# Optimization experiments

Hardware: AMD Instinct MI355X
Metric: run time of the kernel (lower is better)

Reference implementation:

```python
import math
import jax
import jax.numpy as jnp
import numpy as np

LMAX = 6                 # lmax
F8, F2 = 16, 64          # f_out//8, f_out//2 for f_out=128
DIM6 = sum((2 * l + 1) ** 2 for l in range(LMAX + 1))  # 455 = dim of so3_irreps(6)
NA = NB = NG = 16        # SO(3) activation grid (alpha, beta, gamma)
B, T, H, C = 32, 16, 4, 128


def _real_sh(lmax, xyz):
    # real spherical harmonics: (N,3) unit vectors -> (N,(lmax+1)^2), m=-l..l per l
    x, y, z = xyz[:, 0], xyz[:, 1], xyz[:, 2]
    st = np.sqrt(np.clip(1.0 - z * z, 0.0, None))
    phi = np.arctan2(y, x)
    n = xyz.shape[0]
    P = np.zeros((lmax + 1, lmax + 1, n))
    P[0, 0] = 1.0
    for m in range(1, lmax + 1):
        P[m, m] = -(2 * m - 1) * st * P[m - 1, m - 1]
    for m in range(lmax):
        P[m + 1, m] = (2 * m + 1) * z * P[m, m]
    for m in range(lmax + 1):
        for l in range(m + 2, lmax + 1):
            P[l, m] = ((2 * l - 1) * z * P[l - 1, m] - (l + m - 1) * P[l - 2, m]) / (l - m)
    cols = []
    for l in range(lmax + 1):
        for m in range(-l, l + 1):
            am = abs(m)
            K = math.sqrt((2 * l + 1) / (4 * math.pi) * math.factorial(l - am) / math.factorial(l + am))
            if m > 0:
                cols.append(math.sqrt(2.0) * K * np.cos(m * phi) * P[l, m])
            elif m < 0:
                cols.append(math.sqrt(2.0) * K * np.sin(am * phi) * P[l, am])
            else:
                cols.append(K * P[l, 0])
    return np.stack(cols, axis=-1)


def _flat_wigner(lmax, Rs):
    # component-normalized flat real Wigner-D basis: (G,3,3) -> (G, sum_l (2l+1)^2)
    # D_l(R) solved from Y_l(R x) = D_l(R) Y_l(x) by least squares in float64
    rng = np.random.default_rng(0)
    pts = rng.normal(size=(32, 3))
    pts /= np.linalg.norm(pts, axis=1, keepdims=True)
    Y = _real_sh(lmax, pts)                                     # (32,(lmax+1)^2)
    rp = np.einsum('gij,nj->gni', Rs, pts).reshape(-1, 3)
    Yr = _real_sh(lmax, rp).reshape(len(Rs), 32, -1)            # (G,32,(lmax+1)^2)
    blocks = []
    for l in range(lmax + 1):
        d = 2 * l + 1
        o = l * l
        Apinv = np.linalg.pinv(Y[:, o:o + d])                   # (d,32)
        D = np.einsum('kn,gnm->gmk', Apinv, Yr[:, :, o:o + d])  # (G,d,d)
        blocks.append(math.sqrt(d) * D.reshape(len(Rs), d * d))
    return np.concatenate(blocks, axis=-1)


def _rz(a):
    c, s = np.cos(a), np.sin(a)
    z, o = np.zeros_like(a), np.ones_like(a)
    return np.stack([np.stack([c, -s, z], -1), np.stack([s, c, z], -1), np.stack([z, z, o], -1)], -2)


def _ry(a):
    c, s = np.cos(a), np.sin(a)
    z, o = np.zeros_like(a), np.ones_like(a)
    return np.stack([np.stack([c, z, s], -1), np.stack([z, o, z], -1), np.stack([-s, z, c], -1)], -2)


def _so3_grid():
    # ZYZ Euler grid, Gauss-Legendre in beta; rotations (G,3,3) + Haar weights (G,) summing to 1
    nodes, wts = np.polynomial.legendre.leggauss(NB)
    betas = np.arccos(nodes)
    alphas = np.arange(NA) * 2 * np.pi / NA
    gammas = np.arange(NG) * 2 * np.pi / NG
    Aa, Bb, Cg = np.meshgrid(alphas, betas, gammas, indexing='ij')
    Rs = _rz(Aa.ravel()) @ _ry(Bb.ravel()) @ _rz(Cg.ravel())
    w = np.broadcast_to(wts[None, :, None], (NA, NB, NG)).ravel().copy()
    w *= (2 * np.pi / NA) * (2 * np.pi / NG) / (8 * np.pi ** 2)
    return Rs, w


def _ico_rotations():
    # the 60 rotations of the icosahedral group, generated by closure
    phi = (1.0 + 5.0 ** 0.5) / 2.0
    def rot(axis, ang):
        a = np.asarray(axis, dtype=np.float64)
        a = a / np.linalg.norm(a)
        K = np.array([[0.0, -a[2], a[1]], [a[2], 0.0, -a[0]], [-a[1], a[0], 0.0]])
        return np.eye(3) + math.sin(ang) * K + (1.0 - math.cos(ang)) * (K @ K)
    gens = [rot([0.0, 1.0, phi], 2.0 * np.pi / 5.0), rot([0.0, 0.0, 1.0], np.pi)]
    elems = [np.eye(3)]
    seen = {tuple(np.round(np.eye(3), 5).ravel())}
    frontier = list(elems)
    while frontier:
        nxt = []
        for R in frontier:
            for g in gens:
                Q = g @ R
                k = tuple(np.round(Q, 5).ravel())
                if k not in seen:
                    seen.add(k)
                    elems.append(Q)
                    nxt.append(Q)
        frontier = nxt
    return np.stack(elems)


def _equi_linear(xl, wl):
    # e3nn-style per-irrep linear: xl (...,f_in,u,m), wl (f_in,f_out,u,v); fan_in = f_in*u
    fan_in = wl.shape[0] * wl.shape[2]
    return jnp.einsum('...fum,fguv->...gvm', xl, wl) / np.sqrt(fan_in)


def _forward(x, trajectory, w1s, w1v, w2, D_in, D_outw, ico_wigners):
    b, t, _ = trajectory.shape
    # pack '1x0e+3x1e': scalar = traj[...,9], vectors = traj[...,:9]
    s = trajectory[..., 9][..., None, None, None]       # (b,t,f=1,u=1,m=1)
    v = trajectory[..., :9].reshape(b, t, 1, 3, 3)      # (b,t,f=1,u=3,m=3)
    h = jnp.concatenate([_equi_linear(s, w1s).reshape(b, t, F8, 1),
                         _equi_linear(v, w1v).reshape(b, t, F8, 9)], axis=-1)  # (b,t,16,10)
    # SO(3) activation: coeffs -> grid signal -> relu -> coeffs (lmax 1 -> 6)
    sig = jax.nn.relu(jnp.einsum('btci,gi->btcg', h, D_in))
    h = jnp.einsum('btcg,gi->btci', sig, D_outw)        # (b,t,16,455)
    # per-l equivariant linear, f 16 -> 64
    outs = []
    o = 0
    for l in range(LMAX + 1):
        d = 2 * l + 1
        xl = h[..., o:o + d * d].reshape(b, t, F8, d, d)
        outs.append(_equi_linear(xl, w2[l]).reshape(b, t, F2, d * d))
        o += d * d
    traj = jnp.concatenate(outs, axis=-1)               # (b,t,64,455)
    traj = jnp.einsum('bhcj,ij->bhci', traj, ico_wigners)  # sample on ico rotations
    xg = jnp.einsum('bhcj,ij->bhci', x, ico_wigners)
    return xg, traj


def setup_inputs():
    key = jax.random.key(0)
    ks = jax.random.split(key, 11)
    Rs, w = _so3_grid()
    D_in = _flat_wigner(1, Rs).astype(np.float32)                      # (G,10)
    D_outw = (_flat_wigner(LMAX, Rs) * w[:, None]).astype(np.float32)  # (G,455)
    ico = _flat_wigner(LMAX, _ico_rotations()).astype(np.float32)      # (60,455)
    inp = dict(
        x=jax.random.normal(ks[0], (B, H, C, DIM6), jnp.float32),
        trajectory=jax.random.normal(ks[1], (B, T, 10), jnp.float32),
        w1s=jax.random.normal(ks[2], (1, F8, 1, 1), jnp.float32),
        w1v=jax.random.normal(ks[3], (1, F8, 3, 3), jnp.float32),
        D_in=jnp.asarray(D_in),
        D_outw=jnp.asarray(D_outw),
        ico_wigners=jnp.asarray(ico),
    )
    for l in range(LMAX + 1):
        inp['w2_%d' % l] = jax.random.normal(ks[4 + l], (F8, F2, 2 * l + 1, 2 * l + 1), jnp.float32)
    return inp


def reference(x, trajectory, w1s, w1v, w2_0, w2_1, w2_2, w2_3, w2_4, w2_5, w2_6, D_in, D_outw, ico_wigners):
    w2 = [w2_0, w2_1, w2_2, w2_3, w2_4, w2_5, w2_6]
    return _forward(x, trajectory, w1s, w1v, w2, D_in, D_outw, ico_wigners)
```

## Files before the change

### kernel.cpp

```cpp
#include <hip/hip_runtime.h>
#include <math.h>


#define NBT  512
#define F8c  16
#define F2c  64
#define GJ   455
#define GG   4096
#define NICO 60
#define JP   512

typedef short bf16x8 __attribute__((ext_vector_type(8)));
typedef float f32x4  __attribute__((ext_vector_type(4)));
typedef unsigned int u32;
typedef unsigned short ushort;

struct W7 { const float* p[7]; };

__device__ __forceinline__ ushort f2bf(float f) {
  u32 u = __float_as_uint(f);
  return (ushort)((u + 0x7fffu + ((u >> 16) & 1u)) >> 16);
}

__device__ __forceinline__ int sel7(int l, int a0, int a1, int a2, int a3,
                                    int a4, int a5, int a6) {
  int r = a6;
  r = (l == 5) ? a5 : r; r = (l == 4) ? a4 : r; r = (l == 3) ? a3 : r;
  r = (l == 2) ? a2 : r; r = (l == 1) ? a1 : r; r = (l == 0) ? a0 : r;
  return r;
}
__device__ __forceinline__ float sel7f(int l, float a0, float a1, float a2,
                                       float a3, float a4, float a5, float a6) {
  float r = a6;
  r = (l == 5) ? a5 : r; r = (l == 4) ? a4 : r; r = (l == 3) ? a3 : r;
  r = (l == 2) ? a2 : r; r = (l == 1) ? a1 : r; r = (l == 0) ? a0 : r;
  return r;
}

__global__ __launch_bounds__(256) void k_pre(const float* __restrict__ traj,
                                             const float* __restrict__ w1s,
                                             const float* __restrict__ w1v,
                                             const float* __restrict__ ico,
                                             const float* __restrict__ Dout,
                                             W7 w2,
                                             float* __restrict__ h,
                                             ushort* __restrict__ icoB,
                                             ushort* __restrict__ icoBx,
                                             ushort* __restrict__ DoutBT,
                                             ushort* __restrict__ Abuf,
                                             ushort* __restrict__ Bbuf) {
  __shared__ float t[64][65];
  int b = blockIdx.x, tid = threadIdx.x;
  if (b < 2240) {
    ((uint4*)Abuf)[b * 256 + tid] = (uint4){0, 0, 0, 0};
  } else if (b < 2752) {
    int b2 = b - 2240;
    int jt = b2 & 7, kt = b2 >> 3;
    int tx = tid & 63, ty = tid >> 6;
    #pragma unroll
    for (int i = 0; i < 16; ++i) {
      int r = i * 4 + ty, j = jt * 64 + tx;
      t[r][tx] = (j < GJ) ? Dout[(size_t)(kt * 64 + r) * GJ + j] : 0.f;
    }
    __syncthreads();
    #pragma unroll
    for (int i = 0; i < 16; ++i) {
      int jl = i * 4 + ty;
      DoutBT[(size_t)(jt * 64 + jl) * GG + kt * 64 + tx] = f2bf(t[tx][jl]);
    }
  } else if (b < 4992) {
    int ee = (b - 2752) * 256 + tid;
    if (ee < 573440) {
      int l = (ee >= 4096) + (ee >= 16384) + (ee >= 57344) + (ee >= 114688) +
              (ee >= 225280) + (ee >= 360448);
      int base = sel7(l, 0, 4096, 16384, 57344, 114688, 225280, 360448);
      int d    = sel7(l, 1, 3, 5, 7, 9, 11, 13);
      int Kp   = sel7(l, 64, 64, 128, 128, 192, 192, 256);
      int local = ee - base;
      int row = local / Kp, kcol = local - row * Kp;
      int g2 = row / d, v = row - g2 * d;
      ushort val = 0;
      if (kcol < 16 * d) {
        int f = kcol / d, u = kcol - f * d;
        const float* wl = w2.p[l];
        float scl = rsqrtf(16.f * (float)d);
        val = f2bf(wl[(((size_t)f * 64 + g2) * d + u) * d + v] * scl);
      }
      Bbuf[ee] = val;
    }
  } else if (b < 5312) {
    int idx = (b - 4992) * 256 + tid;
    if (idx < NBT * 160) {
      int bt = idx / 160, r = idx % 160, c = r / 10, i = r % 10;
      const float* tr = traj + bt * 10;
      float val;
      if (i == 0) {
        val = tr[9] * w1s[c];
      } else {
        int k = i - 1, v = k / 3, m = k % 3;
        float s = 0.f;
        #pragma unroll
        for (int u = 0; u < 3; ++u) s = fmaf(tr[u * 3 + m], w1v[c * 9 + u * 3 + v], s);
        val = s * 0.57735026918962576f;
      }
      h[idx] = val;
    }
  } else if (b < 5440) {
    int e = (b - 5312) * 256 + tid;
    int i = e >> 9, k = e & 511;
    ushort val = 0;
    if (i < NICO && k < GJ) {
      int l = (k >= 1) + (k >= 10) + (k >= 35) + (k >= 84) + (k >= 165) + (k >= 286);
      int o = sel7(l, 0, 1, 10, 35, 84, 165, 286);
      int d = sel7(l, 1, 3, 5, 7, 9, 11, 13);
      float rcpd = sel7f(l, 1.f, 1.f / 3.f, 0.2f, 1.f / 7.f, 1.f / 9.f,
                         1.f / 11.f, 1.f / 13.f);
      int local = k - o;
      int m = (int)(((float)local + 0.5f) * rcpd);
      int v = local - m * d;
      val = f2bf(ico[i * GJ + o + v * d + m]);
    }
    icoB[e] = val;
  } else {
    int e = (b - 5440) * 256 + tid;
    int i = e >> 9, j = e & 511;
    icoBx[e] = (i < NICO && j < GJ) ? f2bf(ico[i * GJ + j]) : (ushort)0;
  }
}

__global__ __launch_bounds__(256) void k_sig(const float* __restrict__ h,
                                             const float* __restrict__ Din,
                                             ushort* __restrict__ sigb) {
  __shared__ float hs[160];
  int tid = threadIdx.x;
  int mb = blockIdx.y;
  int kt = blockIdx.x;
  if (tid < 160) hs[tid] = h[mb * 160 + tid];
  float dr[80];
  const float4* dp = (const float4*)(Din + (size_t)(kt * 2048 + tid * 8) * 10);
  #pragma unroll
  for (int q = 0; q < 20; ++q) {
    float4 v = dp[q];
    dr[q * 4 + 0] = v.x; dr[q * 4 + 1] = v.y; dr[q * 4 + 2] = v.z; dr[q * 4 + 3] = v.w;
  }
  __syncthreads();
  #pragma unroll
  for (int r = 0; r < 16; ++r) {
    float hv[10];
    #pragma unroll
    for (int i = 0; i < 10; ++i) hv[i] = hs[r * 10 + i];
    bf16x8 o;
    #pragma unroll
    for (int j = 0; j < 8; ++j) {
      float s = 0.f;
      #pragma unroll
      for (int i = 0; i < 10; ++i) s = fmaf(hv[i], dr[j * 10 + i], s);
      o[j] = (short)f2bf(fmaxf(s, 0.f));
    }
    *(bf16x8*)&sigb[((size_t)(mb * 16 + r)) * GG + kt * 2048 + tid * 8] = o;
  }
}

__global__ __launch_bounds__(256) void k_mm2s(const ushort* __restrict__ A,
                                              const ushort* __restrict__ Bm,
                                              float* __restrict__ part) {
  __shared__ __align__(16) short Asb[2][128 * 64];
  __shared__ __align__(16) short Bsb[2][128 * 64];
  int tid = threadIdx.x;
  int lane = tid & 63, wid = tid >> 6;
  int quad = lane >> 4, lr = lane & 15;
  int wm = wid >> 1, wn = wid & 1;
  int bid = blockIdx.x;
  int mb = bid & 63;
  int split = (bid >> 6) & 1;
  int nb = bid >> 7;
  int k0 = split * 2048;

  const ushort* Ab = A + (size_t)mb * 128 * GG + k0;
  const ushort* Bb = Bm + (size_t)nb * 128 * GG + k0;

  f32x4 acc[4][4];
  #pragma unroll
  for (int a = 0; a < 4; ++a)
    #pragma unroll
    for (int b = 0; b < 4; ++b) acc[a][b] = (f32x4){0.f, 0.f, 0.f, 0.f};

  auto stage = [&](int buf, int kc) {
    #pragma unroll
    for (int it = 0; it < 4; ++it) {
      int s0 = (wid * 4 + it) * 64;
      int s = s0 + lane;
      int r = s >> 3, pp = s & 7, p = pp ^ (r & 7);
      __builtin_amdgcn_global_load_lds(
          (const __attribute__((address_space(1))) u32*)(Ab + (size_t)r * GG + kc + p * 8),
          (__attribute__((address_space(3))) u32*)(&Asb[buf][s0 * 8]), 16, 0, 0);
    }
    #pragma unroll
    for (int it = 0; it < 4; ++it) {
      int s0 = (wid * 4 + it) * 64;
      int s = s0 + lane;
      int r = s >> 3, pp = s & 7, p = pp ^ (r & 7);
      __builtin_amdgcn_global_load_lds(
          (const __attribute__((address_space(1))) u32*)(Bb + (size_t)r * GG + kc + p * 8),
          (__attribute__((address_space(3))) u32*)(&Bsb[buf][s0 * 8]), 16, 0, 0);
    }
  };

  stage(0, 0);
  __syncthreads();
  for (int it = 0; it < 32; ++it) {
    int cur = it & 1;
    if (it < 31) stage(cur ^ 1, (it + 1) * 64);
    #pragma unroll
    for (int ks = 0; ks < 2; ++ks) {
      bf16x8 af[4], bv[4];
      #pragma unroll
      for (int mt = 0; mt < 4; ++mt) {
        int ra = wm * 64 + mt * 16 + lr;
        int v = (ks * 4 + quad) ^ (ra & 7);
        af[mt] = *(const bf16x8*)&Asb[cur][(ra * 8 + v) * 8];
      }
      #pragma unroll
      for (int nt = 0; nt < 4; ++nt) {
        int rb = wn * 64 + nt * 16 + lr;
        int v = (ks * 4 + quad) ^ (rb & 7);
        bv[nt] = *(const bf16x8*)&Bsb[cur][(rb * 8 + v) * 8];
      }
      #pragma unroll
      for (int mt = 0; mt < 4; ++mt)
        #pragma unroll
        for (int nt = 0; nt < 4; ++nt)
          acc[mt][nt] = __builtin_amdgcn_mfma_f32_16x16x32_bf16(af[mt], bv[nt], acc[mt][nt], 0, 0, 0);
    }
    __syncthreads();
  }
  #pragma unroll
  for (int mt = 0; mt < 4; ++mt)
    #pragma unroll
    for (int nt = 0; nt < 4; ++nt) {
      int j = nb * 128 + wn * 64 + nt * 16 + lr;
      #pragma unroll
      for (int r = 0; r < 4; ++r) {
        int m = mb * 128 + wm * 64 + mt * 16 + quad * 4 + r;
        part[((size_t)split * 8192 + m) * 512 + j] = acc[mt][nt][r];
      }
    }
}

__global__ __launch_bounds__(256) void k_red(const float* __restrict__ part,
                                             ushort* __restrict__ Abuf) {
  int t = blockIdx.x * 256 + threadIdx.x;
  int e0 = t * 8;
  int m = e0 >> 9, j0 = e0 & 511;
  const float4* p0 = (const float4*)(part + (size_t)m * 512 + j0);
  const float4* p1 = (const float4*)(part + (size_t)(8192 + m) * 512 + j0);
  float4 a0 = p0[0], a1 = p0[1], b0 = p1[0], b1 = p1[1];
  float s[8] = {a0.x + b0.x, a0.y + b0.y, a0.z + b0.z, a0.w + b0.w,
                a1.x + b1.x, a1.y + b1.y, a1.z + b1.z, a1.w + b1.w};
  int btg = m >> 4, f = m & 15;
  #pragma unroll
  for (int jj = 0; jj < 8; ++jj) {
    int j = j0 + jj;
    if (j < GJ) {
      int l = (j >= 1) + (j >= 10) + (j >= 35) + (j >= 84) + (j >= 165) + (j >= 286);
      int o    = sel7(l, 0, 1, 10, 35, 84, 165, 286);
      int d    = sel7(l, 1, 3, 5, 7, 9, 11, 13);
      int Kp   = sel7(l, 64, 64, 128, 128, 192, 192, 256);
      int Aoff = sel7(l, 0, 32768, 131072, 458752, 917504, 1802240, 2883584);
      float rcpd = sel7f(l, 1.f, 1.f / 3.f, 0.2f, 1.f / 7.f, 1.f / 9.f,
                         1.f / 11.f, 1.f / 13.f);
      int jl = j - o;
      int u = (int)(((float)jl + 0.5f) * rcpd);
      int mB = jl - u * d;
      Abuf[(size_t)Aoff + ((size_t)btg * d + mB) * Kp + f * d + u] = f2bf(s[jj]);
    }
  }
}

__global__ __launch_bounds__(256) void k_mm2f(const ushort* __restrict__ A,
                                              const ushort* __restrict__ Bm,
                                              ushort* __restrict__ Abuf) {
  __shared__ __align__(16) short Asb[2][128 * 64];
  __shared__ __align__(16) short Bsb[2][128 * 64];
  int tid = threadIdx.x;
  int lane = tid & 63, wid = tid >> 6;
  int quad = lane >> 4, lr = lane & 15;
  int wm = wid >> 1, wn = wid & 1;
  int bid = blockIdx.x;
  int mb = bid & 63, nb = bid >> 6;
  f32x4 acc[4][4];
  #pragma unroll
  for (int a = 0; a < 4; ++a)
    #pragma unroll
    for (int b = 0; b < 4; ++b) acc[a][b] = (f32x4){0.f, 0.f, 0.f, 0.f};
  const ushort* Ab = A + (size_t)mb * 128 * GG;
  const ushort* Bb = Bm + (size_t)nb * 128 * GG;
  auto stage = [&](int buf, int kc) {
    #pragma unroll
    for (int it = 0; it < 4; ++it) {
      int s0 = (wid * 4 + it) * 64;
      int s = s0 + lane;
      int r = s >> 3, pp = s & 7, p = pp ^ (r & 7);
      __builtin_amdgcn_global_load_lds(
          (const __attribute__((address_space(1))) u32*)(Ab + (size_t)r * GG + kc + p * 8),
          (__attribute__((address_space(3))) u32*)(&Asb[buf][s0 * 8]), 16, 0, 0);
    }
    #pragma unroll
    for (int it = 0; it < 4; ++it) {
      int s0 = (wid * 4 + it) * 64;
      int s = s0 + lane;
      int r = s >> 3, pp = s & 7, p = pp ^ (r & 7);
      __builtin_amdgcn_global_load_lds(
          (const __attribute__((address_space(1))) u32*)(Bb + (size_t)r * GG + kc + p * 8),
          (__attribute__((address_space(3))) u32*)(&Bsb[buf][s0 * 8]), 16, 0, 0);
    }
  };
  stage(0, 0);
  __syncthreads();
  for (int it = 0; it < 64; ++it) {
    int cur = it & 1;
    if (it < 63) stage(cur ^ 1, (it + 1) * 64);
    #pragma unroll
    for (int ks = 0; ks < 2; ++ks) {
      bf16x8 af[4], bvv[4];
      #pragma unroll
      for (int mt = 0; mt < 4; ++mt) {
        int ra = wm * 64 + mt * 16 + lr;
        int v = (ks * 4 + quad) ^ (ra & 7);
        af[mt] = *(const bf16x8*)&Asb[cur][(ra * 8 + v) * 8];
      }
      #pragma unroll
      for (int nt = 0; nt < 4; ++nt) {
        int rb = wn * 64 + nt * 16 + lr;
        int v = (ks * 4 + quad) ^ (rb & 7);
        bvv[nt] = *(const bf16x8*)&Bsb[cur][(rb * 8 + v) * 8];
      }
      #pragma unroll
      for (int mt = 0; mt < 4; ++mt)
        #pragma unroll
        for (int nt = 0; nt < 4; ++nt)
          acc[mt][nt] = __builtin_amdgcn_mfma_f32_16x16x32_bf16(af[mt], bvv[nt], acc[mt][nt], 0, 0, 0);
    }
    __syncthreads();
  }
  #pragma unroll
  for (int nt = 0; nt < 4; ++nt) {
    int j = nb * 128 + wn * 64 + nt * 16 + lr;
    if (j < GJ) {
      int l = (j >= 1) + (j >= 10) + (j >= 35) + (j >= 84) + (j >= 165) + (j >= 286);
      int o    = sel7(l, 0, 1, 10, 35, 84, 165, 286);
      int d    = sel7(l, 1, 3, 5, 7, 9, 11, 13);
      int Kp   = sel7(l, 64, 64, 128, 128, 192, 192, 256);
      int Aoff = sel7(l, 0, 32768, 131072, 458752, 917504, 1802240, 2883584);
      int jl = j - o;
      float rcpd = 1.0f / (float)d;
      int u = (int)(((float)jl + 0.5f) * rcpd);
      int mB = jl - u * d;
      #pragma unroll
      for (int mt = 0; mt < 4; ++mt)
        #pragma unroll
        for (int r = 0; r < 4; ++r) {
          int m = mb * 128 + wm * 64 + mt * 16 + quad * 4 + r;
          int btg = m >> 4, f = m & 15;
          Abuf[(size_t)Aoff + ((size_t)btg * d + mB) * Kp + f * d + u] =
              f2bf(acc[mt][nt][r]);
        }
    }
  }
}

__global__ __launch_bounds__(256) void k_batchX(const ushort* __restrict__ Abuf,
                                                const ushort* __restrict__ Bbuf,
                                                const float* __restrict__ x,
                                                const ushort* __restrict__ icoBx,
                                                ushort* __restrict__ trajbf,
                                                float* __restrict__ xg) {
  __shared__ __align__(16) short As[2][128 * 64];
  __shared__ __align__(16) short Bs[2][128 * 64];
  int bid = blockIdx.x;
  int tid = threadIdx.x;
  int lane = tid & 63, wid = tid >> 6;
  int quad = lane >> 4, lr = lane & 15;
  int wm = wid >> 1, wn = wid & 1;
  f32x4 acc[4][4];
  #pragma unroll
  for (int a = 0; a < 4; ++a)
    #pragma unroll
    for (int b = 0; b < 4; ++b) acc[a][b] = (f32x4){0.f, 0.f, 0.f, 0.f};

  if (bid >= 1008) {
    int mtile = bid - 1008;
    auto loadx = [&](int itk, float* xv) {
      #pragma unroll
      for (int g = 0; g < 4; ++g) {
        int s = g * 256 + tid;
        int r = s >> 3, p8 = s & 7, p = p8 ^ (r & 7);
        const float* xr = x + (size_t)(mtile * 128 + r) * GJ;
        int j0 = itk * 64 + p * 8;
        #pragma unroll
        for (int jj = 0; jj < 8; ++jj) {
          int j = j0 + jj;
          xv[g * 8 + jj] = (j < GJ) ? xr[j] : 0.f;
        }
      }
    };
    auto writex = [&](int buf, const float* xv) {
      #pragma unroll
      for (int g = 0; g < 4; ++g) {
        int s = g * 256 + tid;
        bf16x8 v8;
        #pragma unroll
        for (int jj = 0; jj < 8; ++jj) v8[jj] = (short)f2bf(xv[g * 8 + jj]);
        *(bf16x8*)&As[buf][s * 8] = v8;
      }
    };
    auto stageBx = [&](int buf, int kc) {
      #pragma unroll
      for (int it = 0; it < 2; ++it) {
        int s0 = (wid * 2 + it) * 64;
        int s = s0 + lane;
        int r = s >> 3, p8 = s & 7, p = p8 ^ (r & 7);
        const ushort* gb = icoBx + (size_t)r * JP + kc + p * 8;
        __builtin_amdgcn_global_load_lds(
            (const __attribute__((address_space(1))) u32*)gb,
            (__attribute__((address_space(3))) u32*)(&Bs[buf][s0 * 8]), 16, 0, 0);
      }
    };
    float xv[32];
    loadx(0, xv);
    writex(0, xv);
    stageBx(0, 0);
    __syncthreads();
    for (int it = 0; it < 8; ++it) {
      int cur = it & 1;
      float xn[32];
      if (it < 7) {
        loadx(it + 1, xn);
        stageBx(cur ^ 1, (it + 1) * 64);
      }
      #pragma unroll
      for (int ks = 0; ks < 2; ++ks) {
        bf16x8 af[4], bv[2];
        #pragma unroll
        for (int mt = 0; mt < 4; ++mt) {
          int ra = wm * 64 + mt * 16 + lr;
          int v = (ks * 4 + quad) ^ (ra & 7);
          af[mt] = *(const bf16x8*)&As[cur][(ra * 8 + v) * 8];
        }
        #pragma unroll
        for (int nt = 0; nt < 2; ++nt) {
          int rb = wn * 32 + nt * 16 + lr;
          int v = (ks * 4 + quad) ^ (rb & 7);
          bv[nt] = *(const bf16x8*)&Bs[cur][(rb * 8 + v) * 8];
        }
        #pragma unroll
        for (int mt = 0; mt < 4; ++mt)
          #pragma unroll
          for (int nt = 0; nt < 2; ++nt)
            acc[mt][nt] = __builtin_amdgcn_mfma_f32_16x16x32_bf16(af[mt], bv[nt], acc[mt][nt], 0, 0, 0);
      }
      if (it < 7) writex(cur ^ 1, xn);
      __syncthreads();
    }
    #pragma unroll
    for (int mt = 0; mt < 4; ++mt)
      #pragma unroll
      for (int nt = 0; nt < 2; ++nt) {
        int i = wn * 32 + nt * 16 + lr;
        if (i < NICO) {
          #pragma unroll
          for (int r = 0; r < 4; ++r) {
            int row = mtile * 128 + wm * 64 + mt * 16 + quad * 4 + r;
            xg[(size_t)row * NICO + i] = acc[mt][nt][r];
          }
        }
      }
    return;
  }

  int l = (bid >= 4) + (bid >= 28) + (bid >= 88) + (bid >= 200) +
          (bid >= 380) + (bid >= 644);
  int bbase = sel7(l, 0, 4, 28, 88, 200, 380, 644);
  int d     = sel7(l, 1, 3, 5, 7, 9, 11, 13);
  int Kp    = sel7(l, 64, 64, 128, 128, 192, 192, 256);
  int o     = sel7(l, 0, 1, 10, 35, 84, 165, 286);
  int Aoff  = sel7(l, 0, 32768, 131072, 458752, 917504, 1802240, 2883584);
  int Boff  = sel7(l, 0, 4096, 16384, 57344, 114688, 225280, 360448);
  int ntc   = sel7(l, 1, 2, 3, 4, 5, 6, 7);
  float rcpntc = sel7f(l, 1.f, 0.5f, 1.f / 3.f, 0.25f, 0.2f, 1.f / 6.f, 1.f / 7.f);
  float rcpd   = sel7f(l, 1.f, 1.f / 3.f, 0.2f, 1.f / 7.f, 1.f / 9.f,
                       1.f / 11.f, 1.f / 13.f);
  int t = bid - bbase;
  int mtile = (int)(((float)t + 0.5f) * rcpntc);
  int ntile = t - mtile * ntc;
  int Nl = 64 * d;

  const ushort* Ab = Abuf + Aoff + (size_t)mtile * 128 * Kp;
  const ushort* Bb = Bbuf + Boff + (size_t)ntile * 128 * Kp;

  auto stage = [&](int buf, int kc) {
    #pragma unroll
    for (int it = 0; it < 4; ++it) {
      int s0 = (wid * 4 + it) * 64;
      int s = s0 + lane;
      int r = s >> 3, pp = s & 7, p = pp ^ (r & 7);
      __builtin_amdgcn_global_load_lds(
          (const __attribute__((address_space(1))) u32*)(Ab + (size_t)r * Kp + kc + p * 8),
          (__attribute__((address_space(3))) u32*)(&As[buf][s0 * 8]), 16, 0, 0);
    }
    #pragma unroll
    for (int it = 0; it < 4; ++it) {
      int s0 = (wid * 4 + it) * 64;
      int s = s0 + lane;
      int r = s >> 3, pp = s & 7, p = pp ^ (r & 7);
      __builtin_amdgcn_global_load_lds(
          (const __attribute__((address_space(1))) u32*)(Bb + (size_t)r * Kp + kc + p * 8),
          (__attribute__((address_space(3))) u32*)(&Bs[buf][s0 * 8]), 16, 0, 0);
    }
  };

  int nIter = Kp >> 6;
  stage(0, 0);
  __syncthreads();
  for (int it = 0; it < nIter; ++it) {
    int cur = it & 1;
    if (it + 1 < nIter) stage(cur ^ 1, (it + 1) * 64);
    #pragma unroll
    for (int ks = 0; ks < 2; ++ks) {
      bf16x8 af[4], bv[4];
      #pragma unroll
      for (int mt = 0; mt < 4; ++mt) {
        int ra = wm * 64 + mt * 16 + lr;
        int v = (ks * 4 + quad) ^ (ra & 7);
        af[mt] = *(const bf16x8*)&As[cur][(ra * 8 + v) * 8];
      }
      #pragma unroll
      for (int nt = 0; nt < 4; ++nt) {
        int rb = wn * 64 + nt * 16 + lr;
        int v = (ks * 4 + quad) ^ (rb & 7);
        bv[nt] = *(const bf16x8*)&Bs[cur][(rb * 8 + v) * 8];
      }
      #pragma unroll
      for (int mt = 0; mt < 4; ++mt)
        #pragma unroll
        for (int nt = 0; nt < 4; ++nt)
          acc[mt][nt] = __builtin_amdgcn_mfma_f32_16x16x32_bf16(af[mt], bv[nt], acc[mt][nt], 0, 0, 0);
    }
    __syncthreads();
  }
  #pragma unroll
  for (int nt = 0; nt < 4; ++nt) {
    int Ncol = ntile * 128 + wn * 64 + nt * 16 + lr;
    if (Ncol < Nl) {
      int g2 = (int)(((float)Ncol + 0.5f) * rcpd);
      int v = Ncol - g2 * d;
      #pragma unroll
      for (int mt = 0; mt < 4; ++mt)
        #pragma unroll
        for (int r = 0; r < 4; ++r) {
          int Mrow = mtile * 128 + wm * 64 + mt * 16 + quad * 4 + r;
          int bt = (int)(((float)Mrow + 0.5f) * rcpd);
          int m = Mrow - bt * d;
          trajbf[(size_t)(bt * 64 + g2) * JP + o + m * d + v] = f2bf(acc[mt][nt][r]);
        }
    }
  }
}

__global__ __launch_bounds__(256) void k_icoT(const ushort* __restrict__ trajbf,
                                              const ushort* __restrict__ icoB,
                                              float* __restrict__ trajo) {
  __shared__ __align__(16) short As[2][128 * 64];
  __shared__ __align__(16) short Bs[2][64 * 64];
  int mtile = blockIdx.x;
  int tid = threadIdx.x;
  int lane = tid & 63, wid = tid >> 6;
  int quad = lane >> 4, lr = lane & 15;
  int wm = wid >> 1, wn = wid & 1;
  f32x4 acc[4][2];
  #pragma unroll
  for (int a = 0; a < 4; ++a)
    #pragma unroll
    for (int b = 0; b < 2; ++b) acc[a][b] = (f32x4){0.f, 0.f, 0.f, 0.f};

  auto stage = [&](int buf, int kc) {
    #pragma unroll
    for (int it = 0; it < 4; ++it) {
      int s0 = (wid * 4 + it) * 64;
      int s = s0 + lane;
      int r = s >> 3, p8 = s & 7, p = p8 ^ (r & 7);
      const ushort* ga = trajbf + (size_t)(mtile * 128 + r) * JP + kc + p * 8;
      __builtin_amdgcn_global_load_lds(
          (const __attribute__((address_space(1))) u32*)ga,
          (__attribute__((address_space(3))) u32*)(&As[buf][s0 * 8]), 16, 0, 0);
    }
    #pragma unroll
    for (int it = 0; it < 2; ++it) {
      int s0 = (wid * 2 + it) * 64;
      int s = s0 + lane;
      int r = s >> 3, p8 = s & 7, p = p8 ^ (r & 7);
      const ushort* gb = icoB + (size_t)r * JP + kc + p * 8;
      __builtin_amdgcn_global_load_lds(
          (const __attribute__((address_space(1))) u32*)gb,
          (__attribute__((address_space(3))) u32*)(&Bs[buf][s0 * 8]), 16, 0, 0);
    }
  };

  stage(0, 0);
  __syncthreads();
  for (int it = 0; it < 8; ++it) {
    int cur = it & 1;
    if (it < 7) stage(cur ^ 1, (it + 1) * 64);
    #pragma unroll
    for (int ks = 0; ks < 2; ++ks) {
      bf16x8 af[4], bv[2];
      #pragma unroll
      for (int mt = 0; mt < 4; ++mt) {
        int ra = wm * 64 + mt * 16 + lr;
        int v = (ks * 4 + quad) ^ (ra & 7);
        af[mt] = *(const bf16x8*)&As[cur][(ra * 8 + v) * 8];
      }
      #pragma unroll
      for (int nt = 0; nt < 2; ++nt) {
        int rb = wn * 32 + nt * 16 + lr;
        int v = (ks * 4 + quad) ^ (rb & 7);
        bv[nt] = *(const bf16x8*)&Bs[cur][(rb * 8 + v) * 8];
      }
      #pragma unroll
      for (int mt = 0; mt < 4; ++mt)
        #pragma unroll
        for (int nt = 0; nt < 2; ++nt)
          acc[mt][nt] = __builtin_amdgcn_mfma_f32_16x16x32_bf16(af[mt], bv[nt], acc[mt][nt], 0, 0, 0);
    }
    __syncthreads();
  }
  #pragma unroll
  for (int mt = 0; mt < 4; ++mt)
    #pragma unroll
    for (int nt = 0; nt < 2; ++nt) {
      int i = wn * 32 + nt * 16 + lr;
      if (i < NICO) {
        #pragma unroll
        for (int r = 0; r < 4; ++r) {
          int row = mtile * 128 + wm * 64 + mt * 16 + quad * 4 + r;
          trajo[(size_t)row * NICO + i] = acc[mt][nt][r];
        }
      }
    }
}

extern "C" void kernel_launch(void* const* d_in, const int* in_sizes, int n_in,
                              void* d_out, int out_size, void* d_ws, size_t ws_size,
                              hipStream_t stream) {
  const float *x = nullptr, *traj = nullptr, *w1s = nullptr, *w1v = nullptr;
  const float *Din = nullptr, *Dout = nullptr, *ico = nullptr;
  W7 w2{};
  for (int i = 0; i < n_in; ++i) {
    const float* p = (const float*)d_in[i];
    switch (in_sizes[i]) {
      case 7454720: x = p; break;
      case 5120:    traj = p; break;
      case 16:      w1s = p; break;
      case 144:     w1v = p; break;
      case 40960:   Din = p; break;
      case 1863680: Dout = p; break;
      case 27300:   ico = p; break;
      case 1024:    w2.p[0] = p; break;
      case 9216:    w2.p[1] = p; break;
      case 25600:   w2.p[2] = p; break;
      case 50176:   w2.p[3] = p; break;
      case 82944:   w2.p[4] = p; break;
      case 123904:  w2.p[5] = p; break;
      case 173056:  w2.p[6] = p; break;
      default: break;
    }
  }
  char* wsb = (char*)d_ws;
  float*  h       = (float*)wsb;
  ushort* DoutBT  = (ushort*)(wsb + 327680);
  ushort* icoB    = (ushort*)(wsb + 4521984);
  ushort* icoBx   = (ushort*)(wsb + 4587520);
  ushort* Abuf    = (ushort*)(wsb + 4653056);
  ushort* Bbuf    = (ushort*)(wsb + 13828096);
  ushort* sigb    = (ushort*)(wsb + 14974976);
  ushort* trajbf  = sigb;
  float*  part    = (float*)(wsb + 82083840);
  float* xg    = (float*)d_out;
  float* trajo = (float*)d_out + 983040;

  k_pre<<<dim3(5568), dim3(256), 0, stream>>>(traj, w1s, w1v, ico, Dout, w2,
                                              h, icoB, icoBx, DoutBT, Abuf, Bbuf);
  k_sig<<<dim3(2, 512), dim3(256), 0, stream>>>(h, Din, sigb);
  if (ws_size >= 115638272ULL) {
    k_mm2s<<<dim3(512),  dim3(256), 0, stream>>>(sigb, DoutBT, part);
    k_red <<<dim3(2048), dim3(256), 0, stream>>>(part, Abuf);
  } else {
    k_mm2f<<<dim3(256),  dim3(256), 0, stream>>>(sigb, DoutBT, Abuf);
  }
  k_batchX<<<dim3(1136), dim3(256), 0, stream>>>(Abuf, Bbuf, x, icoBx, trajbf, xg);
  k_icoT  <<<dim3(256),  dim3(256), 0, stream>>>(trajbf, icoB, trajo);
}
```

Measured before the change: 236.0 us.

## Split x projection into bf16 conversion pass and GEMM merged into icoT kernel

The x×ico GEMM tail blocks in k_batchX, which converted fp32 x to bf16 in registers while computing, become lightweight conversion blocks that write bf16 x to a workspace buffer. The GEMM itself moves into k_icoT as 128 extra blocks that share the async global_load_lds staging path with the trajectory GEMM. The aim is to stop long GEMM tail blocks from extending k_batchX and to reuse the more efficient staged pipeline. In exchange it adds an extra bf16 round trip of x through memory and enlarges the workspace.

```diff
diff --git a/kernel.cpp b/kernel.cpp
--- a/kernel.cpp
+++ b/kernel.cpp
@@ -372,13 +372,27 @@
 __global__ __launch_bounds__(256) void k_batchX(const ushort* __restrict__ Abuf,
                                                 const ushort* __restrict__ Bbuf,
                                                 const float* __restrict__ x,
-                                                const ushort* __restrict__ icoBx,
                                                 ushort* __restrict__ trajbf,
-                                                float* __restrict__ xg) {
+                                                ushort* __restrict__ xbf) {
   __shared__ __align__(16) short As[2][128 * 64];
   __shared__ __align__(16) short Bs[2][128 * 64];
   int bid = blockIdx.x;
   int tid = threadIdx.x;
+
+  if (bid >= 1008) {
+    int e0 = ((bid - 1008) * 256 + tid) * 8;
+    int row = e0 >> 9, j0 = e0 & 511;
+    const float* xr = x + (size_t)row * GJ;
+    bf16x8 v8;
+    #pragma unroll
+    for (int jj = 0; jj < 8; ++jj) {
+      int j = j0 + jj;
+      v8[jj] = (j < GJ) ? (short)f2bf(xr[j]) : (short)0;
+    }
+    *(bf16x8*)&xbf[(size_t)row * JP + j0] = v8;
+    return;
+  }
+
   int lane = tid & 63, wid = tid >> 6;
   int quad = lane >> 4, lr = lane & 15;
   int wm = wid >> 1, wn = wid & 1;
@@ -387,96 +401,6 @@
   for (int a = 0; a < 4; ++a)
     #pragma unroll
     for (int b = 0; b < 4; ++b) acc[a][b] = (f32x4){0.f, 0.f, 0.f, 0.f};
-
-  if (bid >= 1008) {
-    int mtile = bid - 1008;
-    auto loadx = [&](int itk, float* xv) {
-      #pragma unroll
-      for (int g = 0; g < 4; ++g) {
-        int s = g * 256 + tid;
-        int r = s >> 3, p8 = s & 7, p = p8 ^ (r & 7);
-        const float* xr = x + (size_t)(mtile * 128 + r) * GJ;
-        int j0 = itk * 64 + p * 8;
-        #pragma unroll
-        for (int jj = 0; jj < 8; ++jj) {
-          int j = j0 + jj;
-          xv[g * 8 + jj] = (j < GJ) ? xr[j] : 0.f;
-        }
-      }
-    };
-    auto writex = [&](int buf, const float* xv) {
-      #pragma unroll
-      for (int g = 0; g < 4; ++g) {
-        int s = g * 256 + tid;
-        bf16x8 v8;
-        #pragma unroll
-        for (int jj = 0; jj < 8; ++jj) v8[jj] = (short)f2bf(xv[g * 8 + jj]);
-        *(bf16x8*)&As[buf][s * 8] = v8;
-      }
-    };
-    auto stageBx = [&](int buf, int kc) {
-      #pragma unroll
-      for (int it = 0; it < 2; ++it) {
-        int s0 = (wid * 2 + it) * 64;
-        int s = s0 + lane;
-        int r = s >> 3, p8 = s & 7, p = p8 ^ (r & 7);
-        const ushort* gb = icoBx + (size_t)r * JP + kc + p * 8;
-        __builtin_amdgcn_global_load_lds(
-            (const __attribute__((address_space(1))) u32*)gb,
-            (__attribute__((address_space(3))) u32*)(&Bs[buf][s0 * 8]), 16, 0, 0);
-      }
-    };
-    float xv[32];
-    loadx(0, xv);
-    writex(0, xv);
-    stageBx(0, 0);
-    __syncthreads();
-    for (int it = 0; it < 8; ++it) {
-      int cur = it & 1;
-      float xn[32];
-      if (it < 7) {
-        loadx(it + 1, xn);
-        stageBx(cur ^ 1, (it + 1) * 64);
-      }
-      #pragma unroll
-      for (int ks = 0; ks < 2; ++ks) {
-        bf16x8 af[4], bv[2];
-        #pragma unroll
-        for (int mt = 0; mt < 4; ++mt) {
-          int ra = wm * 64 + mt * 16 + lr;
-          int v = (ks * 4 + quad) ^ (ra & 7);
-          af[mt] = *(const bf16x8*)&As[cur][(ra * 8 + v) * 8];
-        }
-        #pragma unroll
-        for (int nt = 0; nt < 2; ++nt) {
-          int rb = wn * 32 + nt * 16 + lr;
-          int v = (ks * 4 + quad) ^ (rb & 7);
-          bv[nt] = *(const bf16x8*)&Bs[cur][(rb * 8 + v) * 8];
-        }
-        #pragma unroll
-        for (int mt = 0; mt < 4; ++mt)
-          #pragma unroll
-          for (int nt = 0; nt < 2; ++nt)
-            acc[mt][nt] = __builtin_amdgcn_mfma_f32_16x16x32_bf16(af[mt], bv[nt], acc[mt][nt], 0, 0, 0);
-      }
-      if (it < 7) writex(cur ^ 1, xn);
-      __syncthreads();
-    }
-    #pragma unroll
-    for (int mt = 0; mt < 4; ++mt)
-      #pragma unroll
-      for (int nt = 0; nt < 2; ++nt) {
-        int i = wn * 32 + nt * 16 + lr;
-        if (i < NICO) {
-          #pragma unroll
-          for (int r = 0; r < 4; ++r) {
-            int row = mtile * 128 + wm * 64 + mt * 16 + quad * 4 + r;
-            xg[(size_t)row * NICO + i] = acc[mt][nt][r];
-          }
-        }
-      }
-    return;
-  }
 
   int l = (bid >= 4) + (bid >= 28) + (bid >= 88) + (bid >= 200) +
           (bid >= 380) + (bid >= 644);
@@ -569,14 +493,30 @@
 
 __global__ __launch_bounds__(256) void k_icoT(const ushort* __restrict__ trajbf,
                                               const ushort* __restrict__ icoB,
-                                              float* __restrict__ trajo) {
+                                              const ushort* __restrict__ xbf,
+                                              const ushort* __restrict__ icoBx,
+                                              float* __restrict__ trajo,
+                                              float* __restrict__ xg) {
   __shared__ __align__(16) short As[2][128 * 64];
   __shared__ __align__(16) short Bs[2][64 * 64];
-  int mtile = blockIdx.x;
+  int bid = blockIdx.x;
   int tid = threadIdx.x;
   int lane = tid & 63, wid = tid >> 6;
   int quad = lane >> 4, lr = lane & 15;
   int wm = wid >> 1, wn = wid & 1;
+
+  const ushort* Ap; const ushort* Bp; float* outp;
+  if (bid < 256) {
+    Ap = trajbf + (size_t)bid * 128 * JP;
+    Bp = icoB;
+    outp = trajo + (size_t)bid * 128 * NICO;
+  } else {
+    int m2 = bid - 256;
+    Ap = xbf + (size_t)m2 * 128 * JP;
+    Bp = icoBx;
+    outp = xg + (size_t)m2 * 128 * NICO;
+  }
+
   f32x4 acc[4][2];
   #pragma unroll
   for (int a = 0; a < 4; ++a)
@@ -589,7 +529,7 @@
       int s0 = (wid * 4 + it) * 64;
       int s = s0 + lane;
       int r = s >> 3, p8 = s & 7, p = p8 ^ (r & 7);
-      const ushort* ga = trajbf + (size_t)(mtile * 128 + r) * JP + kc + p * 8;
+      const ushort* ga = Ap + (size_t)r * JP + kc + p * 8;
       __builtin_amdgcn_global_load_lds(
           (const __attribute__((address_space(1))) u32*)ga,
           (__attribute__((address_space(3))) u32*)(&As[buf][s0 * 8]), 16, 0, 0);
@@ -599,7 +539,7 @@
       int s0 = (wid * 2 + it) * 64;
       int s = s0 + lane;
       int r = s >> 3, p8 = s & 7, p = p8 ^ (r & 7);
-      const ushort* gb = icoB + (size_t)r * JP + kc + p * 8;
+      const ushort* gb = Bp + (size_t)r * JP + kc + p * 8;
       __builtin_amdgcn_global_load_lds(
           (const __attribute__((address_space(1))) u32*)gb,
           (__attribute__((address_space(3))) u32*)(&Bs[buf][s0 * 8]), 16, 0, 0);
@@ -642,8 +582,8 @@
       if (i < NICO) {
         #pragma unroll
         for (int r = 0; r < 4; ++r) {
-          int row = mtile * 128 + wm * 64 + mt * 16 + quad * 4 + r;
-          trajo[(size_t)row * NICO + i] = acc[mt][nt][r];
+          int row = wm * 64 + mt * 16 + quad * 4 + r;
+          outp[(size_t)row * NICO + i] = acc[mt][nt][r];
         }
       }
     }
@@ -684,6 +624,7 @@
   ushort* Bbuf    = (ushort*)(wsb + 13828096);
   ushort* sigb    = (ushort*)(wsb + 14974976);
   ushort* trajbf  = sigb;
+  ushort* xbf     = (ushort*)(wsb + 48529408);
   float*  part    = (float*)(wsb + 82083840);
   float* xg    = (float*)d_out;
   float* trajo = (float*)d_out + 983040;
@@ -697,6 +638,7 @@
   } else {
     k_mm2f<<<dim3(256),  dim3(256), 0, stream>>>(sigb, DoutBT, Abuf);
   }
-  k_batchX<<<dim3(1136), dim3(256), 0, stream>>>(Abuf, Bbuf, x, icoBx, trajbf, xg);
-  k_icoT  <<<dim3(256),  dim3(256), 0, stream>>>(trajbf, icoB, trajo);
-}
+  k_batchX<<<dim3(5104), dim3(256), 0, stream>>>(Abuf, Bbuf, x, trajbf, xbf);
+  k_icoT  <<<dim3(384),  dim3(256), 0, stream>>>(trajbf, icoB, xbf, icoBx,
+                                                 trajo, xg);
+}
```

Measured after the change: 241.4 us. +2.3%, slower.
